# Kernel optimization log

Hardware: AMD Instinct MI355X
Metric: run time of the kernel (lower is better)

The kernel has to match this reference:

```python
import jax, jax.numpy as jnp
import numpy as np

N_PTS = 1_000_000
RES = 512
RANK = 48
OUT = 32
INIT_SCALE = 0.1


def _plane_sample(plane, gx, gy):
    """Bilinear grid_sample, align_corners=True, border padding.
    plane: [R, Res, Res] (R=rank); gx, gy: [N] in [-1,1] -> [R, N]."""
    res = plane.shape[-1]
    px = jnp.clip((gx + 1.0) * 0.5 * (res - 1), 0.0, res - 1.0)
    py = jnp.clip((gy + 1.0) * 0.5 * (res - 1), 0.0, res - 1.0)
    x0 = jnp.floor(px).astype(jnp.int32)
    y0 = jnp.floor(py).astype(jnp.int32)
    x1 = jnp.minimum(x0 + 1, res - 1)
    y1 = jnp.minimum(y0 + 1, res - 1)
    wx = px - x0.astype(px.dtype)
    wy = py - y0.astype(py.dtype)
    # gathers: [R, N] each
    v00 = plane[:, y0, x0]
    v01 = plane[:, y0, x1]
    v10 = plane[:, y1, x0]
    v11 = plane[:, y1, x1]
    return (v00 * (1 - wy) * (1 - wx) + v01 * (1 - wy) * wx
            + v10 * wy * (1 - wx) + v11 * wy * wx)


def _line_sample(line, gy):
    """Line is [R, Res] (width dim of size 1 collapses; x coord is 0 -> px=0).
    1-D linear interp along Res with gy in [-1,1] -> [R, N]."""
    res = line.shape[-1]
    py = jnp.clip((gy + 1.0) * 0.5 * (res - 1), 0.0, res - 1.0)
    y0 = jnp.floor(py).astype(jnp.int32)
    y1 = jnp.minimum(y0 + 1, res - 1)
    wy = py - y0.astype(py.dtype)
    return line[:, y0] * (1 - wy) + line[:, y1] * wy


def _geo_forward(coordinates, plane_xy, plane_xz, plane_yz,
                 line_z, line_y, line_x, proj_w, proj_b):
    coords = coordinates * 2.0 - 1.0  # [N, 3] in [-1, 1]
    cx, cy, cz = coords[:, 0], coords[:, 1], coords[:, 2]
    vm = (_plane_sample(plane_xy, cx, cy) * _line_sample(line_z, cz)
          + _plane_sample(plane_xz, cx, cz) * _line_sample(line_y, cy)
          + _plane_sample(plane_yz, cy, cz) * _line_sample(line_x, cx))  # [R, N]
    # projection: [N, R] @ [R, OUT] + b
    return vm.T @ proj_w.T + proj_b


def setup_inputs() -> dict:
    key = jax.random.key(0)
    ks = jax.random.split(key, 9)
    return {
        "coordinates": jax.random.uniform(ks[0], (N_PTS, 3), dtype=jnp.float32),
        "plane_xy": jax.random.normal(ks[1], (RANK, RES, RES), jnp.float32) * INIT_SCALE,
        "plane_xz": jax.random.normal(ks[2], (RANK, RES, RES), jnp.float32) * INIT_SCALE,
        "plane_yz": jax.random.normal(ks[3], (RANK, RES, RES), jnp.float32) * INIT_SCALE,
        "line_z": jax.random.normal(ks[4], (RANK, RES), jnp.float32) * INIT_SCALE,
        "line_y": jax.random.normal(ks[5], (RANK, RES), jnp.float32) * INIT_SCALE,
        "line_x": jax.random.normal(ks[6], (RANK, RES), jnp.float32) * INIT_SCALE,
        "proj_w": jax.random.normal(ks[7], (OUT, RANK), jnp.float32) * INIT_SCALE,
        "proj_b": jnp.zeros((OUT,), jnp.float32),
    }


def reference(coordinates, plane_xy, plane_xz, plane_yz,
              line_z, line_y, line_x, proj_w, proj_b):
    return _geo_forward(coordinates, plane_xy, plane_xz, plane_yz,
                        line_z, line_y, line_x, proj_w, proj_b)
```

## Files before the change

### kernel.cpp

```cpp
#include <hip/hip_runtime.h>
#include <stdint.h>

#define RES      512
#define TEXELS   (RES * RES)
#define NPTS     1000000
#define RANK     48
#define ODIM     32
#define TEXB     96
#define PLANE_WS ((size_t)TEXELS * TEXB)
#define LINE_WS  ((size_t)RES * TEXB)
#define PPB      64
#define VMS      52

typedef unsigned int u32;

__device__ __forceinline__ float lobf(u32 u) { return __uint_as_float(u << 16); }
__device__ __forceinline__ float hibf(u32 u) { return __uint_as_float(u & 0xffff0000u); }

__device__ __forceinline__ u32 pkbf(float a, float b) {
    u32 x = __float_as_uint(a), y = __float_as_uint(b);
    u32 xr = (x + 0x7fffu + ((x >> 16) & 1u)) >> 16;
    u32 yr = (y + 0x7fffu + ((y >> 16) & 1u)) & 0xffff0000u;
    return xr | yr;
}

__global__ __launch_bounds__(256) void transpose_planes(
    const float* __restrict__ p0, const float* __restrict__ p1,
    const float* __restrict__ p2, char* __restrict__ ws)
{
    int t2 = blockIdx.x * 256 + threadIdx.x;
    int plane = blockIdx.y;
    const float* src = (plane == 0) ? p0 : ((plane == 1) ? p1 : p2);
    int tex = t2 * 2;
    u32 r0[24], r1[24];
#pragma unroll
    for (int m = 0; m < 24; ++m) {
        float2 a = *(const float2*)(src + (size_t)(2 * m) * TEXELS + tex);
        float2 b = *(const float2*)(src + (size_t)(2 * m + 1) * TEXELS + tex);
        r0[m] = pkbf(a.x, b.x);
        r1[m] = pkbf(a.y, b.y);
    }
    char* dst = ws + (size_t)plane * PLANE_WS + (size_t)tex * TEXB;
#pragma unroll
    for (int k = 0; k < 6; ++k) {
        *(uint4*)(dst + 16 * k) =
            make_uint4(r0[4 * k], r0[4 * k + 1], r0[4 * k + 2], r0[4 * k + 3]);
        *(uint4*)(dst + TEXB + 16 * k) =
            make_uint4(r1[4 * k], r1[4 * k + 1], r1[4 * k + 2], r1[4 * k + 3]);
    }
}

__global__ __launch_bounds__(256) void transpose_lines(
    const float* __restrict__ lz, const float* __restrict__ ly,
    const float* __restrict__ lx, char* __restrict__ ws)
{
    int id = blockIdx.x * 256 + threadIdx.x;
    int line = id >> 9;
    int pos = id & (RES - 1);
    const float* src = (line == 0) ? lz : ((line == 1) ? ly : lx);
    char* dst = ws + 3 * PLANE_WS + (size_t)line * LINE_WS + (size_t)pos * TEXB;
#pragma unroll
    for (int k = 0; k < 6; ++k) {
        uint4 q;
        q.x = pkbf(src[(8 * k + 0) * RES + pos], src[(8 * k + 1) * RES + pos]);
        q.y = pkbf(src[(8 * k + 2) * RES + pos], src[(8 * k + 3) * RES + pos]);
        q.z = pkbf(src[(8 * k + 4) * RES + pos], src[(8 * k + 5) * RES + pos]);
        q.w = pkbf(src[(8 * k + 6) * RES + pos], src[(8 * k + 7) * RES + pos]);
        *(uint4*)(dst + 16 * k) = q;
    }
}

__device__ __forceinline__ void prep1(float g, int& i0, int& i1, float& w) {
    float p = fminf(fmaxf((g + 1.f) * 0.5f * 511.f, 0.f), 511.f);
    float fp = floorf(p);
    i0 = (int)fp;
    i1 = min(i0 + 1, RES - 1);
    w = p - fp;
}

__global__ __launch_bounds__(512, 4) void geo_main(
    const float* __restrict__ coords, const char* __restrict__ ws,
    const float* __restrict__ W, const float* __restrict__ Bb,
    float* __restrict__ out)
{
    __shared__ float vm_lds[PPB * VMS];

    int tid = threadIdx.x;
    int ptL = tid >> 3;
    int c = tid & 7;
    int pt = blockIdx.x * PPB + ptL;

    float gx = coords[3 * pt + 0] * 2.f - 1.f;
    float gy = coords[3 * pt + 1] * 2.f - 1.f;
    float gz = coords[3 * pt + 2] * 2.f - 1.f;

    int x0, x1, y0, y1, z0, z1;
    float wx, wy, wz;
    prep1(gx, x0, x1, wx);
    prep1(gy, y0, y1, wy);
    prep1(gz, z0, z1, wz);

    const char* pxy = ws;
    const char* pxz = ws + PLANE_WS;
    const char* pyz = ws + 2 * PLANE_WS;
    const char* lzb = ws + 3 * PLANE_WS;
    const char* lyb = lzb + LINE_WS;
    const char* lxb = lyb + LINE_WS;

    u32 co = 12u * (u32)c;

    u32 q[12][3], le[3][3], lf[3][3];
    {
        u32 offs[12];
        offs[0] = (u32)(y0 * RES + x0) * TEXB + co;
        offs[1] = (u32)(y0 * RES + x1) * TEXB + co;
        offs[2] = (u32)(y1 * RES + x0) * TEXB + co;
        offs[3] = (u32)(y1 * RES + x1) * TEXB + co;
        offs[4] = (u32)(z0 * RES + x0) * TEXB + co;
        offs[5] = (u32)(z0 * RES + x1) * TEXB + co;
        offs[6] = (u32)(z1 * RES + x0) * TEXB + co;
        offs[7] = (u32)(z1 * RES + x1) * TEXB + co;
        offs[8]  = (u32)(z0 * RES + y0) * TEXB + co;
        offs[9]  = (u32)(z0 * RES + y1) * TEXB + co;
        offs[10] = (u32)(z1 * RES + y0) * TEXB + co;
        offs[11] = (u32)(z1 * RES + y1) * TEXB + co;
        const char* bases[3] = { pxy, pxz, pyz };
#pragma unroll
        for (int p = 0; p < 3; ++p) {
#pragma unroll
            for (int k = 0; k < 4; ++k) {
                const u32* s = (const u32*)(bases[p] + offs[4 * p + k]);
                q[4 * p + k][0] = s[0];
                q[4 * p + k][1] = s[1];
                q[4 * p + k][2] = s[2];
            }
        }
        const char* lb[3] = { lzb, lyb, lxb };
        u32 l0[3] = { (u32)z0 * TEXB + co, (u32)y0 * TEXB + co, (u32)x0 * TEXB + co };
        u32 l1[3] = { (u32)z1 * TEXB + co, (u32)y1 * TEXB + co, (u32)x1 * TEXB + co };
#pragma unroll
        for (int p = 0; p < 3; ++p) {
            const u32* s0 = (const u32*)(lb[p] + l0[p]);
            const u32* s1 = (const u32*)(lb[p] + l1[p]);
            le[p][0] = s0[0]; le[p][1] = s0[1]; le[p][2] = s0[2];
            lf[p][0] = s1[0]; lf[p][1] = s1[1]; lf[p][2] = s1[2];
        }
    }

    float pw[3][4];
    pw[0][0] = (1.f - wy) * (1.f - wx); pw[0][1] = (1.f - wy) * wx;
    pw[0][2] = wy * (1.f - wx);         pw[0][3] = wy * wx;
    pw[1][0] = (1.f - wz) * (1.f - wx); pw[1][1] = (1.f - wz) * wx;
    pw[1][2] = wz * (1.f - wx);         pw[1][3] = wz * wx;
    pw[2][0] = (1.f - wz) * (1.f - wy); pw[2][1] = (1.f - wz) * wy;
    pw[2][2] = wz * (1.f - wy);         pw[2][3] = wz * wy;
    float lw[3] = { wz, wy, wx };

    float vm[6] = { 0.f, 0.f, 0.f, 0.f, 0.f, 0.f };
#pragma unroll
    for (int p = 0; p < 3; ++p) {
        float s0 = pw[p][0], s1 = pw[p][1], s2 = pw[p][2], s3 = pw[p][3];
        float il = 1.f - lw[p], wl = lw[p];
#pragma unroll
        for (int d = 0; d < 3; ++d) {
            u32 a = q[4 * p + 0][d], b = q[4 * p + 1][d];
            u32 cc = q[4 * p + 2][d], dd = q[4 * p + 3][d];
            float slo = s0 * lobf(a) + s1 * lobf(b) + s2 * lobf(cc) + s3 * lobf(dd);
            float shi = s0 * hibf(a) + s1 * hibf(b) + s2 * hibf(cc) + s3 * hibf(dd);
            float llo = il * lobf(le[p][d]) + wl * lobf(lf[p][d]);
            float lhi = il * hibf(le[p][d]) + wl * hibf(lf[p][d]);
            vm[2 * d + 0] = fmaf(slo, llo, vm[2 * d + 0]);
            vm[2 * d + 1] = fmaf(shi, lhi, vm[2 * d + 1]);
        }
    }

    float* vr = vm_lds + ptL * VMS + 6 * c;
    *(float2*)(vr + 0) = make_float2(vm[0], vm[1]);
    *(float2*)(vr + 2) = make_float2(vm[2], vm[3]);
    *(float2*)(vr + 4) = make_float2(vm[4], vm[5]);

    __syncthreads();

    int wav = __builtin_amdgcn_readfirstlane(tid >> 6);
    int lane = tid & 63;
    int ob = wav * 4;

    const float* vmrow = vm_lds + lane * VMS;
    float4 bb = *(const float4*)(Bb + ob);
    float a0 = bb.x, a1 = bb.y, a2 = bb.z, a3 = bb.w;
#pragma unroll 4
    for (int k = 0; k < 12; ++k) {
        float4 v = *(const float4*)(vmrow + 4 * k);
        float4 w0 = *(const float4*)(W + (ob + 0) * RANK + 4 * k);
        float4 w1 = *(const float4*)(W + (ob + 1) * RANK + 4 * k);
        float4 w2 = *(const float4*)(W + (ob + 2) * RANK + 4 * k);
        float4 w3 = *(const float4*)(W + (ob + 3) * RANK + 4 * k);
        a0 = fmaf(v.x, w0.x, a0); a0 = fmaf(v.y, w0.y, a0);
        a0 = fmaf(v.z, w0.z, a0); a0 = fmaf(v.w, w0.w, a0);
        a1 = fmaf(v.x, w1.x, a1); a1 = fmaf(v.y, w1.y, a1);
        a1 = fmaf(v.z, w1.z, a1); a1 = fmaf(v.w, w1.w, a1);
        a2 = fmaf(v.x, w2.x, a2); a2 = fmaf(v.y, w2.y, a2);
        a2 = fmaf(v.z, w2.z, a2); a2 = fmaf(v.w, w2.w, a2);
        a3 = fmaf(v.x, w3.x, a3); a3 = fmaf(v.y, w3.y, a3);
        a3 = fmaf(v.z, w3.z, a3); a3 = fmaf(v.w, w3.w, a3);
    }
    size_t optr = (size_t)(blockIdx.x * PPB + lane) * ODIM + ob;
    *(float4*)(out + optr) = make_float4(a0, a1, a2, a3);
}

extern "C" void kernel_launch(void* const* d_in, const int* in_sizes, int n_in,
                              void* d_out, int out_size, void* d_ws, size_t ws_size,
                              hipStream_t stream) {
    const float* coords = (const float*)d_in[0];
    const float* pxy = (const float*)d_in[1];
    const float* pxz = (const float*)d_in[2];
    const float* pyz = (const float*)d_in[3];
    const float* lz = (const float*)d_in[4];
    const float* ly = (const float*)d_in[5];
    const float* lx = (const float*)d_in[6];
    const float* W = (const float*)d_in[7];
    const float* Bb = (const float*)d_in[8];
    float* out = (float*)d_out;
    char* ws = (char*)d_ws;

    dim3 gt(TEXELS / 2 / 256, 3);
    transpose_planes<<<gt, 256, 0, stream>>>(pxy, pxz, pyz, ws);
    transpose_lines<<<6, 256, 0, stream>>>(lz, ly, lx, ws);

    geo_main<<<NPTS / PPB, 512, 0, stream>>>(coords, ws, W, Bb, out);
}
```

Baseline: 512.3 us.

## Stage plane transpose through LDS and pad texel stride to 128 bytes

The plane transpose kernel now reads one float per thread per rank pair, packs to bf16 into a shared-memory tile, and writes the transposed texels out as contiguous 16-byte chunks, giving coalesced writes. All kernels are templated on the texel stride, and when the workspace is large enough a 128-byte padded stride is used instead of 96. The padded stride aligns each texel's gather to cache-line boundaries in the main sampling kernel. In exchange it uses about a third more workspace and memory traffic for the transposed planes.

Result: faster. 483.5 us (-5.6%).

```diff
diff --git a/kernel.cpp b/kernel.cpp
--- a/kernel.cpp
+++ b/kernel.cpp
@@ -6,11 +6,10 @@
 #define NPTS     1000000
 #define RANK     48
 #define ODIM     32
-#define TEXB     96
-#define PLANE_WS ((size_t)TEXELS * TEXB)
-#define LINE_WS  ((size_t)RES * TEXB)
 #define PPB      64
 #define VMS      52
+#define TT       128
+#define TS       25
 
 typedef unsigned int u32;
 
@@ -24,32 +23,47 @@
     return xr | yr;
 }
 
+template <int TEXB>
 __global__ __launch_bounds__(256) void transpose_planes(
     const float* __restrict__ p0, const float* __restrict__ p1,
     const float* __restrict__ p2, char* __restrict__ ws)
 {
-    int t2 = blockIdx.x * 256 + threadIdx.x;
+    __shared__ u32 lds[TT * TS + 8];
+
+    int t = threadIdx.x;
+    int base = blockIdx.x * TT;
     int plane = blockIdx.y;
     const float* src = (plane == 0) ? p0 : ((plane == 1) ? p1 : p2);
-    int tex = t2 * 2;
-    u32 r0[24], r1[24];
-#pragma unroll
-    for (int m = 0; m < 24; ++m) {
-        float2 a = *(const float2*)(src + (size_t)(2 * m) * TEXELS + tex);
-        float2 b = *(const float2*)(src + (size_t)(2 * m + 1) * TEXELS + tex);
-        r0[m] = pkbf(a.x, b.x);
-        r1[m] = pkbf(a.y, b.y);
-    }
-    char* dst = ws + (size_t)plane * PLANE_WS + (size_t)tex * TEXB;
-#pragma unroll
-    for (int k = 0; k < 6; ++k) {
-        *(uint4*)(dst + 16 * k) =
-            make_uint4(r0[4 * k], r0[4 * k + 1], r0[4 * k + 2], r0[4 * k + 3]);
-        *(uint4*)(dst + TEXB + 16 * k) =
-            make_uint4(r1[4 * k], r1[4 * k + 1], r1[4 * k + 2], r1[4 * k + 3]);
-    }
-}
-
+
+    int t7 = t & (TT - 1);
+    int half = t >> 7;
+#pragma unroll
+    for (int j = 0; j < 12; ++j) {
+        int d = half * 12 + j;
+        float a = src[(size_t)(2 * d) * TEXELS + base + t7];
+        float b = src[(size_t)(2 * d + 1) * TEXELS + base + t7];
+        lds[t7 * TS + d] = pkbf(a, b);
+    }
+    __syncthreads();
+
+    char* outp = ws + (size_t)plane * TEXELS * TEXB + (size_t)base * TEXB;
+    constexpr int NS = TT * TEXB / (16 * 256);
+#pragma unroll
+    for (int s = 0; s < NS; ++s) {
+        u32 o = (u32)(s * 256 + t) * 16u;
+        u32 texel, rem;
+        if (TEXB == 128) { texel = o >> 7; rem = o & 127u; }
+        else {
+            texel = ((o >> 5) * 43691u) >> 17;
+            rem = o - texel * 96u;
+        }
+        u32 dw = texel * TS + (rem >> 2);
+        uint4 q = make_uint4(lds[dw], lds[dw + 1], lds[dw + 2], lds[dw + 3]);
+        *(uint4*)(outp + o) = q;
+    }
+}
+
+template <int TEXB>
 __global__ __launch_bounds__(256) void transpose_lines(
     const float* __restrict__ lz, const float* __restrict__ ly,
     const float* __restrict__ lx, char* __restrict__ ws)
@@ -58,7 +72,8 @@
     int line = id >> 9;
     int pos = id & (RES - 1);
     const float* src = (line == 0) ? lz : ((line == 1) ? ly : lx);
-    char* dst = ws + 3 * PLANE_WS + (size_t)line * LINE_WS + (size_t)pos * TEXB;
+    char* dst = ws + (size_t)3 * TEXELS * TEXB + (size_t)line * RES * TEXB
+                   + (size_t)pos * TEXB;
 #pragma unroll
     for (int k = 0; k < 6; ++k) {
         uint4 q;
@@ -78,6 +93,7 @@
     w = p - fp;
 }
 
+template <int TEXB>
 __global__ __launch_bounds__(512, 4) void geo_main(
     const float* __restrict__ coords, const char* __restrict__ ws,
     const float* __restrict__ W, const float* __restrict__ Bb,
@@ -100,12 +116,14 @@
     prep1(gy, y0, y1, wy);
     prep1(gz, z0, z1, wz);
 
+    const size_t PW = (size_t)TEXELS * TEXB;
+    const size_t LW = (size_t)RES * TEXB;
     const char* pxy = ws;
-    const char* pxz = ws + PLANE_WS;
-    const char* pyz = ws + 2 * PLANE_WS;
-    const char* lzb = ws + 3 * PLANE_WS;
-    const char* lyb = lzb + LINE_WS;
-    const char* lxb = lyb + LINE_WS;
+    const char* pxz = ws + PW;
+    const char* pyz = ws + 2 * PW;
+    const char* lzb = ws + 3 * PW;
+    const char* lyb = lzb + LW;
+    const char* lxb = lyb + LW;
 
     u32 co = 12u * (u32)c;
 
@@ -208,6 +226,17 @@
     *(float4*)(out + optr) = make_float4(a0, a1, a2, a3);
 }
 
+template <int TEXB>
+static void launch_all(const float* coords, const float* pxy, const float* pxz,
+                       const float* pyz, const float* lz, const float* ly,
+                       const float* lx, const float* W, const float* Bb,
+                       float* out, char* ws, hipStream_t stream) {
+    dim3 gt(TEXELS / TT, 3);
+    transpose_planes<TEXB><<<gt, 256, 0, stream>>>(pxy, pxz, pyz, ws);
+    transpose_lines<TEXB><<<6, 256, 0, stream>>>(lz, ly, lx, ws);
+    geo_main<TEXB><<<NPTS / PPB, 512, 0, stream>>>(coords, ws, W, Bb, out);
+}
+
 extern "C" void kernel_launch(void* const* d_in, const int* in_sizes, int n_in,
                               void* d_out, int out_size, void* d_ws, size_t ws_size,
                               hipStream_t stream) {
@@ -223,9 +252,9 @@
     float* out = (float*)d_out;
     char* ws = (char*)d_ws;
 
-    dim3 gt(TEXELS / 2 / 256, 3);
-    transpose_planes<<<gt, 256, 0, stream>>>(pxy, pxz, pyz, ws);
-    transpose_lines<<<6, 256, 0, stream>>>(lz, ly, lx, ws);
-
-    geo_main<<<NPTS / PPB, 512, 0, stream>>>(coords, ws, W, Bb, out);
-}
+    size_t need128 = (size_t)3 * TEXELS * 128 + (size_t)3 * RES * 128;
+    if (ws_size >= need128)
+        launch_all<128>(coords, pxy, pxz, pyz, lz, ly, lx, W, Bb, out, ws, stream);
+    else
+        launch_all<96>(coords, pxy, pxz, pyz, lz, ly, lx, W, Bb, out, ws, stream);
+}
```
